# Optimization experiments

Hardware: AMD Instinct MI355X
Metric: run time of the kernel (lower is better)

Reference implementation:

```python
import jax, jax.numpy as jnp
import numpy as np
from jax import lax

N_WIRES = 4
BN_EPS = 1e-5


def _conv2d_same(x, w, b):
    # x: [B,C,H,W], w: [O,I,3,3] -> 'SAME' padding == padding=1 for k=3
    y = lax.conv_general_dilated(x, w, window_strides=(1, 1), padding='SAME',
                                 dimension_numbers=('NCHW', 'OIHW', 'NCHW'))
    return y + b[None, :, None, None]


def _maxpool2(x):
    return lax.reduce_window(x, -jnp.inf, lax.max,
                             window_dimensions=(1, 1, 2, 2),
                             window_strides=(1, 1, 2, 2), padding='VALID')


def setup_inputs() -> dict:
    key = jax.random.key(0)
    ks = jax.random.split(key, 12)
    B = 8192
    x = jax.random.normal(ks[0], (B, 1, 28, 28), dtype=jnp.float32)
    params = jax.random.normal(ks[1], (B, N_WIRES), dtype=jnp.float32)  # per-sample circuit params
    conv1_w = jax.random.normal(ks[2], (8, 1, 3, 3), dtype=jnp.float32) * 0.1
    conv1_b = jnp.zeros((8,), jnp.float32)
    conv2_w = jax.random.normal(ks[3], (16, 8, 3, 3), dtype=jnp.float32) * 0.1
    conv2_b = jnp.zeros((16,), jnp.float32)
    qkv_w = jax.random.normal(ks[4], (3 * N_WIRES, 16 * 7 * 7), dtype=jnp.float32) * 0.03
    qkv_b = jnp.zeros((3 * N_WIRES,), jnp.float32)
    out_w = jax.random.normal(ks[5], (4, N_WIRES), dtype=jnp.float32) * 0.3
    out_b = jnp.zeros((4,), jnp.float32)
    bn_gamma = jnp.ones((4,), jnp.float32)
    bn_beta = jnp.zeros((4,), jnp.float32)
    return dict(x=x, params=params, conv1_w=conv1_w, conv1_b=conv1_b,
                conv2_w=conv2_w, conv2_b=conv2_b, qkv_w=qkv_w, qkv_b=qkv_b,
                out_w=out_w, out_b=out_b, bn_gamma=bn_gamma, bn_beta=bn_beta)


def reference(x, params, conv1_w, conv1_b, conv2_w, conv2_b,
              qkv_w, qkv_b, out_w, out_b, bn_gamma, bn_beta):
    # conv feature extractor: 28 -> 14 -> 7
    f = _maxpool2(jax.nn.relu(_conv2d_same(x, conv1_w, conv1_b)))
    f = _maxpool2(jax.nn.relu(_conv2d_same(f, conv2_w, conv2_b)))
    f_flat = f.reshape(f.shape[0], -1)                     # [B, 784]
    qkv = f_flat @ qkv_w.T + qkv_b                         # [B, 12]
    q, k, v = jnp.split(qkv, 3, axis=1)                    # each [B, 4]
    # Quantum circuit (4 qubits): RX(params[i]); RZ((q+k)[i]); CNOT chain; <Z_i>.
    # RZ is diagonal and commutes with every Z-string observable, so it drops out.
    # Heisenberg evolution through CNOT(0,1),CNOT(1,2),CNOT(2,3) gives
    # <Z_i> = prod_{j<=i} cos(params[j])  (vectorized over the batch).
    _ = q + k  # the circuit input; provably does not affect the expvals
    logits = jnp.cumprod(jnp.cos(params), axis=1)          # [B, 4]
    attn = jax.nn.softmax(logits, axis=1)
    out = attn * v                                         # [B, 4]
    out = out @ out_w.T + out_b                            # [B, 4]
    # BatchNorm1d in training mode: biased batch statistics
    mu = jnp.mean(out, axis=0)
    var = jnp.mean((out - mu) ** 2, axis=0)
    return (out - mu) / jnp.sqrt(var + BN_EPS) * bn_gamma + bn_beta
```

## Files before the change

### kernel.cpp

```cpp
#include <hip/hip_runtime.h>

#define BATCH 8192

typedef __fp16 h2 __attribute__((ext_vector_type(2)));
union H2U { unsigned u; h2 h; };
__device__ __forceinline__ h2 asH2(unsigned v) { H2U t; t.u = v; return t.h; }

__global__ __launch_bounds__(256) void prep(const float* __restrict__ c2w,
                                            unsigned* __restrict__ w2h) {
    int i = blockIdx.x * 256 + threadIdx.x;
    if (i < 576) {
        int oc  = i & 15;
        int t   = i >> 4;
        int icp = t & 3;
        int tap = t >> 2;
        float lo = c2w[oc * 72 + (2 * icp) * 9 + tap];
        float hi = c2w[oc * 72 + (2 * icp + 1) * 9 + tap];
        H2U u; u.h = __builtin_amdgcn_cvt_pkrtz(lo, hi);
        w2h[i] = u.u;
    }
}

__global__ __launch_bounds__(256, 4) void fused_fwd(
    const float* __restrict__ x,
    const float* __restrict__ params,
    const float* __restrict__ c1w,
    const float* __restrict__ c1b,
    const float* __restrict__ c2b,
    const float* __restrict__ qkvw,
    const float* __restrict__ qkvb,
    const float* __restrict__ outw,
    const float* __restrict__ outb,
    const unsigned* __restrict__ w2h,
    float* __restrict__ pre)
{
    __shared__ __align__(16) float lds[5216];
    float*    xs    = lds;
    float*    c2out = lds;
    unsigned* p1h   = (unsigned*)(lds + 3136);
    float*    p2    = lds + 4416;
    float*    vred  = lds + 5200;

    const int tid = threadIdx.x;
    const int b = blockIdx.x;

    for (int i = tid; i < 900; i += 256) {
        int h = i / 30, w = i - h * 30;
        float v = 0.f;
        if (h >= 1 && h <= 28 && w >= 1 && w <= 28)
            v = x[b * 784 + (h - 1) * 28 + (w - 1)];
        xs[i] = v;
    }
    for (int i = tid; i < 1280; i += 256) p1h[i] = 0u;
    __syncthreads();

    {
        const int pos = tid < 196 ? tid : 195;
        const int ph = pos / 14, pw = pos - ph * 14;
        const float* base = &xs[(2 * ph) * 30 + 2 * pw];
        float in[4][4];
        #pragma unroll
        for (int r = 0; r < 4; ++r)
            #pragma unroll
            for (int c = 0; c < 4; ++c)
                in[r][c] = base[r * 30 + c];
        float o[8];
        #pragma unroll
        for (int oc = 0; oc < 8; ++oc) {
            float m = 0.f;
            #pragma unroll
            for (int dh = 0; dh < 2; ++dh)
                #pragma unroll
                for (int dw = 0; dw < 2; ++dw) {
                    float a = c1b[oc];
                    #pragma unroll
                    for (int r = 0; r < 3; ++r)
                        #pragma unroll
                        for (int c = 0; c < 3; ++c)
                            a += in[dh + r][dw + c] * c1w[oc * 9 + r * 3 + c];
                    m = fmaxf(m, a);
                }
            o[oc] = m;
        }
        if (tid < 196) {
            const int obase = ((ph + 1) * 16 + (pw + 1)) * 5;
            H2U u0, u1, u2, u3;
            u0.h = __builtin_amdgcn_cvt_pkrtz(o[0], o[1]);
            u1.h = __builtin_amdgcn_cvt_pkrtz(o[2], o[3]);
            u2.h = __builtin_amdgcn_cvt_pkrtz(o[4], o[5]);
            u3.h = __builtin_amdgcn_cvt_pkrtz(o[6], o[7]);
            p1h[obase + 0] = u0.u;
            p1h[obase + 1] = u1.u;
            p1h[obase + 2] = u2.u;
            p1h[obase + 3] = u3.u;
        }
    }
    __syncthreads();

    {
        const int pos = tid < 196 ? tid : 195;
        const int h = pos / 14, w = pos - h * 14;

        float a0  = c2b[0],  a1  = c2b[1],  a2  = c2b[2],  a3  = c2b[3];
        float a4  = c2b[4],  a5  = c2b[5],  a6  = c2b[6],  a7  = c2b[7];
        float a8  = c2b[8],  a9  = c2b[9],  a10 = c2b[10], a11 = c2b[11];
        float a12 = c2b[12], a13 = c2b[13], a14 = c2b[14], a15 = c2b[15];

        const uint4* wp = (const uint4*)w2h;
        #pragma unroll 1
        for (int dh = 0; dh < 3; ++dh) {
            #pragma unroll 1
            for (int dw = 0; dw < 3; ++dw) {
                const int ibase = ((h + dh) * 16 + (w + dw)) * 5;
                #pragma unroll 1
                for (int icp = 0; icp < 4; ++icp) {
                    const h2 iv = asH2(p1h[ibase + icp]);
                    const uint4 wA = wp[0];
                    const uint4 wB = wp[1];
                    const uint4 wC = wp[2];
                    const uint4 wD = wp[3];
                    a0  = __builtin_amdgcn_fdot2(iv, asH2(wA.x), a0,  false);
                    a1  = __builtin_amdgcn_fdot2(iv, asH2(wA.y), a1,  false);
                    a2  = __builtin_amdgcn_fdot2(iv, asH2(wA.z), a2,  false);
                    a3  = __builtin_amdgcn_fdot2(iv, asH2(wA.w), a3,  false);
                    a4  = __builtin_amdgcn_fdot2(iv, asH2(wB.x), a4,  false);
                    a5  = __builtin_amdgcn_fdot2(iv, asH2(wB.y), a5,  false);
                    a6  = __builtin_amdgcn_fdot2(iv, asH2(wB.z), a6,  false);
                    a7  = __builtin_amdgcn_fdot2(iv, asH2(wB.w), a7,  false);
                    a8  = __builtin_amdgcn_fdot2(iv, asH2(wC.x), a8,  false);
                    a9  = __builtin_amdgcn_fdot2(iv, asH2(wC.y), a9,  false);
                    a10 = __builtin_amdgcn_fdot2(iv, asH2(wC.z), a10, false);
                    a11 = __builtin_amdgcn_fdot2(iv, asH2(wC.w), a11, false);
                    a12 = __builtin_amdgcn_fdot2(iv, asH2(wD.x), a12, false);
                    a13 = __builtin_amdgcn_fdot2(iv, asH2(wD.y), a13, false);
                    a14 = __builtin_amdgcn_fdot2(iv, asH2(wD.z), a14, false);
                    a15 = __builtin_amdgcn_fdot2(iv, asH2(wD.w), a15, false);
                    wp += 4;
                }
            }
        }
        if (tid < 196) {
            c2out[0  * 196 + pos] = fmaxf(a0,  0.f);
            c2out[1  * 196 + pos] = fmaxf(a1,  0.f);
            c2out[2  * 196 + pos] = fmaxf(a2,  0.f);
            c2out[3  * 196 + pos] = fmaxf(a3,  0.f);
            c2out[4  * 196 + pos] = fmaxf(a4,  0.f);
            c2out[5  * 196 + pos] = fmaxf(a5,  0.f);
            c2out[6  * 196 + pos] = fmaxf(a6,  0.f);
            c2out[7  * 196 + pos] = fmaxf(a7,  0.f);
            c2out[8  * 196 + pos] = fmaxf(a8,  0.f);
            c2out[9  * 196 + pos] = fmaxf(a9,  0.f);
            c2out[10 * 196 + pos] = fmaxf(a10, 0.f);
            c2out[11 * 196 + pos] = fmaxf(a11, 0.f);
            c2out[12 * 196 + pos] = fmaxf(a12, 0.f);
            c2out[13 * 196 + pos] = fmaxf(a13, 0.f);
            c2out[14 * 196 + pos] = fmaxf(a14, 0.f);
            c2out[15 * 196 + pos] = fmaxf(a15, 0.f);
        }
    }
    __syncthreads();

    for (int it = tid; it < 784; it += 256) {
        int c = it / 49, r = it - c * 49;
        int ph = r / 7, pw = r - ph * 7;
        const float* pb = &c2out[c * 196 + (2 * ph) * 14 + 2 * pw];
        p2[it] = fmaxf(fmaxf(pb[0], pb[1]), fmaxf(pb[14], pb[15]));
    }
    __syncthreads();

    float v0 = 0.f, v1 = 0.f, v2 = 0.f, v3 = 0.f;
    if (tid < 196) {
        float4 f  = *(const float4*)&p2[tid * 4];
        float4 a0 = ((const float4*)&qkvw[8 * 784])[tid];
        float4 a1 = ((const float4*)&qkvw[9 * 784])[tid];
        float4 a2 = ((const float4*)&qkvw[10 * 784])[tid];
        float4 a3 = ((const float4*)&qkvw[11 * 784])[tid];
        v0 = f.x * a0.x + f.y * a0.y + f.z * a0.z + f.w * a0.w;
        v1 = f.x * a1.x + f.y * a1.y + f.z * a1.z + f.w * a1.w;
        v2 = f.x * a2.x + f.y * a2.y + f.z * a2.z + f.w * a2.w;
        v3 = f.x * a3.x + f.y * a3.y + f.z * a3.z + f.w * a3.w;
    }
    #pragma unroll
    for (int off = 32; off > 0; off >>= 1) {
        v0 += __shfl_xor(v0, off);
        v1 += __shfl_xor(v1, off);
        v2 += __shfl_xor(v2, off);
        v3 += __shfl_xor(v3, off);
    }
    if ((tid & 63) == 0) {
        const int wv = tid >> 6;
        vred[wv * 4 + 0] = v0; vred[wv * 4 + 1] = v1;
        vred[wv * 4 + 2] = v2; vred[wv * 4 + 3] = v3;
    }
    __syncthreads();

    if (tid < 4) {
        float vv[4];
        #pragma unroll
        for (int j = 0; j < 4; ++j)
            vv[j] = vred[0 + j] + vred[4 + j] + vred[8 + j] + vred[12 + j]
                  + qkvb[8 + j];

        float lg[4];
        float run = 1.f;
        #pragma unroll
        for (int j = 0; j < 4; ++j) { run *= cosf(params[b * 4 + j]); lg[j] = run; }
        float mx = fmaxf(fmaxf(lg[0], lg[1]), fmaxf(lg[2], lg[3]));
        float e[4], s = 0.f;
        #pragma unroll
        for (int j = 0; j < 4; ++j) { e[j] = expf(lg[j] - mx); s += e[j]; }
        float inv = 1.f / s;

        float t = outb[tid];
        #pragma unroll
        for (int j = 0; j < 4; ++j) t += outw[tid * 4 + j] * (e[j] * inv * vv[j]);
        pre[b * 4 + tid] = t;
    }
}

__global__ __launch_bounds__(256) void bn_final(
    const float* __restrict__ pre, const float* __restrict__ gamma,
    const float* __restrict__ beta, float* __restrict__ out)
{
    __shared__ float red[4][8];
    const int tid = threadIdx.x;
    const float4* pre4 = (const float4*)pre;

    float4 s = make_float4(0.f, 0.f, 0.f, 0.f);
    float4 q = make_float4(0.f, 0.f, 0.f, 0.f);
    for (int i = tid; i < 8192; i += 256) {
        float4 v = pre4[i];
        s.x += v.x; s.y += v.y; s.z += v.z; s.w += v.w;
        q.x += v.x * v.x; q.y += v.y * v.y; q.z += v.z * v.z; q.w += v.w * v.w;
    }
    #pragma unroll
    for (int off = 32; off > 0; off >>= 1) {
        s.x += __shfl_xor(s.x, off); s.y += __shfl_xor(s.y, off);
        s.z += __shfl_xor(s.z, off); s.w += __shfl_xor(s.w, off);
        q.x += __shfl_xor(q.x, off); q.y += __shfl_xor(q.y, off);
        q.z += __shfl_xor(q.z, off); q.w += __shfl_xor(q.w, off);
    }
    if ((tid & 63) == 0) {
        const int wv = tid >> 6;
        red[wv][0] = s.x; red[wv][1] = s.y; red[wv][2] = s.z; red[wv][3] = s.w;
        red[wv][4] = q.x; red[wv][5] = q.y; red[wv][6] = q.z; red[wv][7] = q.w;
    }
    __syncthreads();

    float mu[4], inv[4];
    #pragma unroll
    for (int c = 0; c < 4; ++c) {
        float ts = red[0][c] + red[1][c] + red[2][c] + red[3][c];
        float tq = red[0][4 + c] + red[1][4 + c] + red[2][4 + c] + red[3][4 + c];
        float m = ts * (1.f / 8192.f);
        mu[c] = m;
        inv[c] = rsqrtf(tq * (1.f / 8192.f) - m * m + 1e-5f);
    }

    if (tid < 64) {
        const int i = blockIdx.x * 64 + tid;
        float4 v = pre4[i];
        float4 g  = *(const float4*)gamma;
        float4 be = *(const float4*)beta;
        float4 o;
        o.x = (v.x - mu[0]) * inv[0] * g.x + be.x;
        o.y = (v.y - mu[1]) * inv[1] * g.y + be.y;
        o.z = (v.z - mu[2]) * inv[2] * g.z + be.z;
        o.w = (v.w - mu[3]) * inv[3] * g.w + be.w;
        ((float4*)out)[i] = o;
    }
}

extern "C" void kernel_launch(void* const* d_in, const int* in_sizes, int n_in,
                              void* d_out, int out_size, void* d_ws, size_t ws_size,
                              hipStream_t stream) {
    const float* x      = (const float*)d_in[0];
    const float* params = (const float*)d_in[1];
    const float* c1w    = (const float*)d_in[2];
    const float* c1b    = (const float*)d_in[3];
    const float* c2w    = (const float*)d_in[4];
    const float* c2b    = (const float*)d_in[5];
    const float* qkvw   = (const float*)d_in[6];
    const float* qkvb   = (const float*)d_in[7];
    const float* outw   = (const float*)d_in[8];
    const float* outb   = (const float*)d_in[9];
    const float* gamma  = (const float*)d_in[10];
    const float* beta   = (const float*)d_in[11];

    unsigned* w2h = (unsigned*)d_ws;
    float*    pre = (float*)d_ws + 1024;

    prep<<<3, 256, 0, stream>>>(c2w, w2h);
    fused_fwd<<<BATCH, 256, 0, stream>>>(x, params, c1w, c1b, c2b,
                                         qkvw, qkvb, outw, outb, w2h, pre);
    bn_final<<<128, 256, 0, stream>>>(pre, gamma, beta, (float*)d_out);
}
```

Measured before the change: 178.2 us.

## Run conv2 as im2col GEMM on MFMA 16x16x32 f16 instructions

Replaces the per-thread fdot2 loop over the 3x3x8 conv2 taps with an explicit im2col staging of each output position's 72-element fp16 patch (padded to 96) in LDS. Four waves then issue mfma_f32_16x16x32_f16 across 13 position tiles, with weights preloaded into registers. The prep kernel repacks weights into a K-padded 96x16 B-operand layout, and the conv2 output is stored position-major with stride 17 to reduce bank conflicts. This raises LDS use to about 47KB per block, which may lower occupancy, and adds an extra staging pass and barrier.

```diff
diff --git a/kernel.cpp b/kernel.cpp
--- a/kernel.cpp
+++ b/kernel.cpp
@@ -3,19 +3,23 @@
 #define BATCH 8192
 
 typedef __fp16 h2 __attribute__((ext_vector_type(2)));
+typedef __fp16 h8 __attribute__((ext_vector_type(8)));
+typedef float f32x4 __attribute__((ext_vector_type(4)));
 union H2U { unsigned u; h2 h; };
-__device__ __forceinline__ h2 asH2(unsigned v) { H2U t; t.u = v; return t.h; }
+union U4H8 { uint4 u; h8 h; };
 
 __global__ __launch_bounds__(256) void prep(const float* __restrict__ c2w,
                                             unsigned* __restrict__ w2h) {
     int i = blockIdx.x * 256 + threadIdx.x;
-    if (i < 576) {
-        int oc  = i & 15;
-        int t   = i >> 4;
-        int icp = t & 3;
-        int tap = t >> 2;
-        float lo = c2w[oc * 72 + (2 * icp) * 9 + tap];
-        float hi = c2w[oc * 72 + (2 * icp + 1) * 9 + tap];
+    if (i < 768) {
+        int oc = i / 48, kp = i - oc * 48;
+        int k0 = 2 * kp;
+        int tap = k0 >> 3, ic0 = k0 & 7;
+        float lo = 0.f, hi = 0.f;
+        if (tap < 9) {
+            lo = c2w[oc * 72 + ic0 * 9 + tap];
+            hi = c2w[oc * 72 + (ic0 + 1) * 9 + tap];
+        }
         H2U u; u.h = __builtin_amdgcn_cvt_pkrtz(lo, hi);
         w2h[i] = u.u;
     }
@@ -34,15 +38,25 @@
     const unsigned* __restrict__ w2h,
     float* __restrict__ pre)
 {
-    __shared__ __align__(16) float lds[5216];
-    float*    xs    = lds;
-    float*    c2out = lds;
-    unsigned* p1h   = (unsigned*)(lds + 3136);
-    float*    p2    = lds + 4416;
-    float*    vred  = lds + 5200;
+    __shared__ __align__(16) float lds[11856];
+    float*    xs   = lds;
+    unsigned* Pu   = (unsigned*)lds;
+    float*    c2o  = lds;
+    unsigned* p1h  = (unsigned*)(lds + 10816);
+    float*    p2   = lds + 10816;
+    float*    vred = lds + 11840;
 
     const int tid = threadIdx.x;
     const int b = blockIdx.x;
+    const int lane = tid & 63;
+    const int lane15 = lane & 15;
+    const int g = lane >> 4;
+
+    U4H8 bf0, bf1, bf2;
+    bf0.u = ((const uint4*)w2h)[lane15 * 12 + 0 + g];
+    bf1.u = ((const uint4*)w2h)[lane15 * 12 + 4 + g];
+    bf2.u = ((const uint4*)w2h)[lane15 * 12 + 8 + g];
+    const float bias16 = c2b[lane15];
 
     for (int i = tid; i < 900; i += 256) {
         int h = i / 30, w = i - h * 30;
@@ -51,7 +65,7 @@
             v = x[b * 784 + (h - 1) * 28 + (w - 1)];
         xs[i] = v;
     }
-    for (int i = tid; i < 1280; i += 256) p1h[i] = 0u;
+    ((uint4*)p1h)[tid] = make_uint4(0u, 0u, 0u, 0u);
     __syncthreads();
 
     {
@@ -83,88 +97,78 @@
             o[oc] = m;
         }
         if (tid < 196) {
-            const int obase = ((ph + 1) * 16 + (pw + 1)) * 5;
             H2U u0, u1, u2, u3;
             u0.h = __builtin_amdgcn_cvt_pkrtz(o[0], o[1]);
             u1.h = __builtin_amdgcn_cvt_pkrtz(o[2], o[3]);
             u2.h = __builtin_amdgcn_cvt_pkrtz(o[4], o[5]);
             u3.h = __builtin_amdgcn_cvt_pkrtz(o[6], o[7]);
-            p1h[obase + 0] = u0.u;
-            p1h[obase + 1] = u1.u;
-            p1h[obase + 2] = u2.u;
-            p1h[obase + 3] = u3.u;
+            ((uint4*)p1h)[(ph + 1) * 16 + (pw + 1)] =
+                make_uint4(u0.u, u1.u, u2.u, u3.u);
         }
     }
     __syncthreads();
 
     {
-        const int pos = tid < 196 ? tid : 195;
-        const int h = pos / 14, w = pos - h * 14;
-
-        float a0  = c2b[0],  a1  = c2b[1],  a2  = c2b[2],  a3  = c2b[3];
-        float a4  = c2b[4],  a5  = c2b[5],  a6  = c2b[6],  a7  = c2b[7];
-        float a8  = c2b[8],  a9  = c2b[9],  a10 = c2b[10], a11 = c2b[11];
-        float a12 = c2b[12], a13 = c2b[13], a14 = c2b[14], a15 = c2b[15];
-
-        const uint4* wp = (const uint4*)w2h;
-        #pragma unroll 1
-        for (int dh = 0; dh < 3; ++dh) {
-            #pragma unroll 1
-            for (int dw = 0; dw < 3; ++dw) {
-                const int ibase = ((h + dh) * 16 + (w + dw)) * 5;
-                #pragma unroll 1
-                for (int icp = 0; icp < 4; ++icp) {
-                    const h2 iv = asH2(p1h[ibase + icp]);
-                    const uint4 wA = wp[0];
-                    const uint4 wB = wp[1];
-                    const uint4 wC = wp[2];
-                    const uint4 wD = wp[3];
-                    a0  = __builtin_amdgcn_fdot2(iv, asH2(wA.x), a0,  false);
-                    a1  = __builtin_amdgcn_fdot2(iv, asH2(wA.y), a1,  false);
-                    a2  = __builtin_amdgcn_fdot2(iv, asH2(wA.z), a2,  false);
-                    a3  = __builtin_amdgcn_fdot2(iv, asH2(wA.w), a3,  false);
-                    a4  = __builtin_amdgcn_fdot2(iv, asH2(wB.x), a4,  false);
-                    a5  = __builtin_amdgcn_fdot2(iv, asH2(wB.y), a5,  false);
-                    a6  = __builtin_amdgcn_fdot2(iv, asH2(wB.z), a6,  false);
-                    a7  = __builtin_amdgcn_fdot2(iv, asH2(wB.w), a7,  false);
-                    a8  = __builtin_amdgcn_fdot2(iv, asH2(wC.x), a8,  false);
-                    a9  = __builtin_amdgcn_fdot2(iv, asH2(wC.y), a9,  false);
-                    a10 = __builtin_amdgcn_fdot2(iv, asH2(wC.z), a10, false);
-                    a11 = __builtin_amdgcn_fdot2(iv, asH2(wC.w), a11, false);
-                    a12 = __builtin_amdgcn_fdot2(iv, asH2(wD.x), a12, false);
-                    a13 = __builtin_amdgcn_fdot2(iv, asH2(wD.y), a13, false);
-                    a14 = __builtin_amdgcn_fdot2(iv, asH2(wD.z), a14, false);
-                    a15 = __builtin_amdgcn_fdot2(iv, asH2(wD.w), a15, false);
-                    wp += 4;
-                }
+        const uint4 z4 = make_uint4(0u, 0u, 0u, 0u);
+        if (tid < 196) {
+            const int h = tid / 14, w = tid - 14 * (tid / 14);
+            uint4* dst = (uint4*)(Pu + tid * 52);
+            #pragma unroll
+            for (int t = 0; t < 9; ++t) {
+                const int dh = t / 3, dw = t - 3 * (t / 3);
+                dst[t] = ((const uint4*)p1h)[(h + dh) * 16 + (w + dw)];
             }
-        }
-        if (tid < 196) {
-            c2out[0  * 196 + pos] = fmaxf(a0,  0.f);
-            c2out[1  * 196 + pos] = fmaxf(a1,  0.f);
-            c2out[2  * 196 + pos] = fmaxf(a2,  0.f);
-            c2out[3  * 196 + pos] = fmaxf(a3,  0.f);
-            c2out[4  * 196 + pos] = fmaxf(a4,  0.f);
-            c2out[5  * 196 + pos] = fmaxf(a5,  0.f);
-            c2out[6  * 196 + pos] = fmaxf(a6,  0.f);
-            c2out[7  * 196 + pos] = fmaxf(a7,  0.f);
-            c2out[8  * 196 + pos] = fmaxf(a8,  0.f);
-            c2out[9  * 196 + pos] = fmaxf(a9,  0.f);
-            c2out[10 * 196 + pos] = fmaxf(a10, 0.f);
-            c2out[11 * 196 + pos] = fmaxf(a11, 0.f);
-            c2out[12 * 196 + pos] = fmaxf(a12, 0.f);
-            c2out[13 * 196 + pos] = fmaxf(a13, 0.f);
-            c2out[14 * 196 + pos] = fmaxf(a14, 0.f);
-            c2out[15 * 196 + pos] = fmaxf(a15, 0.f);
+            dst[9] = z4; dst[10] = z4; dst[11] = z4;
+        } else if (tid < 208) {
+            uint4* dst = (uint4*)(Pu + tid * 52);
+            #pragma unroll
+            for (int t = 0; t < 12; ++t) dst[t] = z4;
+        }
+    }
+    __syncthreads();
+
+    const int wv = tid >> 6;
+    f32x4 acc[4];
+    #pragma unroll
+    for (int t = 0; t < 4; ++t) acc[t] = (f32x4){0.f, 0.f, 0.f, 0.f};
+    #pragma unroll
+    for (int t = 0; t < 4; ++t) {
+        const int tile = wv * 4 + t;
+        if (tile < 13) {
+            const char* abase = (const char*)Pu
+                              + (tile * 16 + lane15) * 208 + g * 16;
+            U4H8 a0, a1, a2;
+            a0.u = *(const uint4*)(abase);
+            a1.u = *(const uint4*)(abase + 64);
+            a2.u = *(const uint4*)(abase + 128);
+            acc[t] = __builtin_amdgcn_mfma_f32_16x16x32_f16(a0.h, bf0.h, acc[t], 0, 0, 0);
+            acc[t] = __builtin_amdgcn_mfma_f32_16x16x32_f16(a1.h, bf1.h, acc[t], 0, 0, 0);
+            acc[t] = __builtin_amdgcn_mfma_f32_16x16x32_f16(a2.h, bf2.h, acc[t], 0, 0, 0);
+        }
+    }
+    __syncthreads();
+
+    #pragma unroll
+    for (int t = 0; t < 4; ++t) {
+        const int tile = wv * 4 + t;
+        if (tile < 13) {
+            #pragma unroll
+            for (int r = 0; r < 4; ++r) {
+                const int pos = tile * 16 + g * 4 + r;
+                if (pos < 196)
+                    c2o[pos * 17 + lane15] = fmaxf(acc[t][r] + bias16, 0.f);
+            }
         }
     }
     __syncthreads();
 
     for (int it = tid; it < 784; it += 256) {
-        int c = it / 49, r = it - c * 49;
-        int ph = r / 7, pw = r - ph * 7;
-        const float* pb = &c2out[c * 196 + (2 * ph) * 14 + 2 * pw];
-        p2[it] = fmaxf(fmaxf(pb[0], pb[1]), fmaxf(pb[14], pb[15]));
+        int oc = it / 49, r = it - oc * 49;
+        int ph = r / 7, pw = r - 7 * (r / 7);
+        int pos0 = (2 * ph) * 14 + 2 * pw;
+        float m = fmaxf(fmaxf(c2o[pos0 * 17 + oc], c2o[(pos0 + 1) * 17 + oc]),
+                        fmaxf(c2o[(pos0 + 14) * 17 + oc], c2o[(pos0 + 15) * 17 + oc]));
+        p2[it] = m;
     }
     __syncthreads();
 
@@ -188,7 +192,6 @@
         v3 += __shfl_xor(v3, off);
     }
     if ((tid & 63) == 0) {
-        const int wv = tid >> 6;
         vred[wv * 4 + 0] = v0; vred[wv * 4 + 1] = v1;
         vred[wv * 4 + 2] = v2; vred[wv * 4 + 3] = v3;
     }
@@ -260,13 +263,13 @@
     if (tid < 64) {
         const int i = blockIdx.x * 64 + tid;
         float4 v = pre4[i];
-        float4 g  = *(const float4*)gamma;
+        float4 gm = *(const float4*)gamma;
         float4 be = *(const float4*)beta;
         float4 o;
-        o.x = (v.x - mu[0]) * inv[0] * g.x + be.x;
-        o.y = (v.y - mu[1]) * inv[1] * g.y + be.y;
-        o.z = (v.z - mu[2]) * inv[2] * g.z + be.z;
-        o.w = (v.w - mu[3]) * inv[3] * g.w + be.w;
+        o.x = (v.x - mu[0]) * inv[0] * gm.x + be.x;
+        o.y = (v.y - mu[1]) * inv[1] * gm.y + be.y;
+        o.z = (v.z - mu[2]) * inv[2] * gm.z + be.z;
+        o.w = (v.w - mu[3]) * inv[3] * gm.w + be.w;
         ((float4*)out)[i] = o;
     }
 }
```

Result: slower. 206.0 us (+15.6%).
